# Kernel tuning notes

Hardware: AMD Instinct MI355X
Metric: run time of the kernel (lower is better)

## Reference

```python
import jax, jax.numpy as jnp
import numpy as np

B, N, DIM_IN, DIM, DIM_C, RES, PAD, NBLK = 4, 32768, 3, 128, 128, 64, 0.1, 5
R2 = RES * RES
PLANES = ((0, 2), (0, 1), (1, 2))  # xz, xy, yz as in ConvONet


def setup_inputs() -> dict:
    key = jax.random.key(0)
    ks = jax.random.split(key, 8)
    x = jax.random.uniform(ks[0], (B, N, DIM_IN), minval=-0.55, maxval=0.55, dtype=jnp.float32)
    w = lambda k, sh: (jax.random.normal(k, sh, dtype=jnp.float32) * 0.02)
    return {
        "x": x,
        "stem_w": w(ks[1], (DIM_IN, 2 * DIM)), "stem_b": jnp.zeros((2 * DIM,), jnp.float32),
        "blk_fc0_w": w(ks[2], (NBLK, 2 * DIM, DIM)), "blk_fc0_b": jnp.zeros((NBLK, DIM), jnp.float32),
        "blk_fc1_w": w(ks[3], (NBLK, DIM, DIM)), "blk_fc1_b": jnp.zeros((NBLK, DIM), jnp.float32),
        "blk_sc_w": w(ks[4], (NBLK, 2 * DIM, DIM)), "blk_sc_b": jnp.zeros((NBLK, DIM), jnp.float32),
        "fc_c_w": w(ks[5], (DIM, DIM_C)), "fc_c_b": jnp.zeros((DIM_C,), jnp.float32),
    }


def _tri_indices(xyz):
    # per-plane flat grid index, ConvONet-style normalization with padding
    idxs = []
    for (a, b) in PLANES:
        p = xyz[..., (a, b)] / (1.0 + PAD + 1e-3) + 0.5
        p = jnp.clip(p, 0.0, 1.0 - 1e-6)
        ij = jnp.clip((p * RES).astype(jnp.int32), 0, RES - 1)
        idxs.append(ij[..., 0] + RES * ij[..., 1])  # (B, N)
    return idxs


def _scatter(c, idx, reduction):
    # c: (B, N, D), idx: (B, N) -> (B, R2, D)
    b, n, d = c.shape
    seg = (idx + jnp.arange(b, dtype=idx.dtype)[:, None] * R2).reshape(-1)
    flat = c.reshape(b * n, d)
    if reduction == "max":
        out = jax.ops.segment_max(flat, seg, num_segments=b * R2)
        out = jnp.where(jnp.isfinite(out), out, jnp.zeros((), c.dtype))  # empty cells -> 0
    else:  # mean
        s = jax.ops.segment_sum(flat, seg, num_segments=b * R2)
        cnt = jax.ops.segment_sum(jnp.ones((b * n, 1), c.dtype), seg, num_segments=b * R2)
        out = s / jnp.maximum(cnt, 1.0)
    return out.reshape(b, R2, d)


def _pool_local(h, idxs):
    # scatter-max into each triplane, gather back per-point, sum over the 3 planes
    out = jnp.zeros_like(h)
    for idx in idxs:
        grid = _scatter(h, idx, "max")                       # (B, R2, D)
        out = out + jnp.take_along_axis(grid, idx[..., None], axis=1)
    return out


def _block(h, w0, b0, w1, b1, ws, bs):
    # pre-activation residual MLP (ResnetBlockFC)
    net = jax.nn.relu(h) @ w0 + b0
    dx = jax.nn.relu(net) @ w1 + b1
    return h @ ws + bs + dx


def reference(x, stem_w, stem_b, blk_fc0_w, blk_fc0_b, blk_fc1_w, blk_fc1_b,
              blk_sc_w, blk_sc_b, fc_c_w, fc_c_b):
    xyz = x[..., :3]
    idxs = _tri_indices(xyz)
    h = x @ stem_w + stem_b                                  # (B, N, 2*DIM)
    h = _block(h, blk_fc0_w[0], blk_fc0_b[0], blk_fc1_w[0], blk_fc1_b[0], blk_sc_w[0], blk_sc_b[0])
    for i in range(1, NBLK):
        h = jnp.concatenate([h, _pool_local(h, idxs)], axis=-1)
        h = _block(h, blk_fc0_w[i], blk_fc0_b[i], blk_fc1_w[i], blk_fc1_b[i], blk_sc_w[i], blk_sc_b[i])
    c = h @ fc_c_w + fc_c_b                                  # (B, N, DIM_C)
    tri = jnp.stack([_scatter(c, idx, "mean") for idx in idxs])  # (3, B, R2, DIM_C)
    # flat index = i + RES*j -> reshape gives (j, i); move channels to front
    tri = tri.reshape(3, B, RES, RES, DIM_C).transpose(0, 1, 4, 2, 3)  # (3, B, DIM_C, RES, RES)
    return (xyz, c, tri)
```

## Files before the change

### kernel.cpp

```cpp
#include <hip/hip_runtime.h>
#include <hip/hip_bf16.h>

#define B_   4
#define NPTS 32768
#define BN   131072
#define RES  64
#define R2   4096
#define DIM  128
#define K2   256
#define NBLK 5
#define NSEG (3*B_*R2)

typedef __bf16 bf16x8 __attribute__((ext_vector_type(8)));
typedef float  f32x16 __attribute__((ext_vector_type(16)));
typedef unsigned int uintv4 __attribute__((ext_vector_type(4)));

#define MFMA(a,b,c) __builtin_amdgcn_mfma_f32_32x32x16_bf16((a),(b),(c),0,0,0)

#define O_IDX  0
#define O_CNT  (O_IDX + BN*16)
#define O_OFF  (O_CNT + NSEG*4)
#define O_WOFF (O_OFF + NSEG*4)
#define O_LIST (O_WOFF + NSEG*4)
#define O_H    (O_LIST + 3*BN*4)
#define O_GRID (O_H + BN*DIM*2)
#define O_W    (O_GRID + NSEG*DIM*2)
#define WBLK_ELEMS 81920

#define OUT_C_OFF   393216
#define OUT_TRI_OFF 17170432

__device__ __forceinline__ unsigned short f2bf(float f){
  unsigned int u = __float_as_uint(f);
  return (unsigned short)((u + 0x7fffu + ((u >> 16) & 1u)) >> 16);
}
__device__ __forceinline__ float bflo(unsigned int u){ return __uint_as_float(u << 16); }
__device__ __forceinline__ float bfhi(unsigned int u){ return __uint_as_float(u & 0xffff0000u); }
__device__ __forceinline__ int coord_bin(float u){
  float p = u / 1.101f + 0.5f;
  p = fminf(fmaxf(p, 0.0f), (float)(1.0 - 1e-6));
  int i = (int)(p * 64.0f);
  return i < 0 ? 0 : (i > 63 ? 63 : i);
}
__device__ __forceinline__ unsigned int pk_relu(unsigned int a){
  unsigned int r, z = 0;
  asm("v_pk_max_f16 %0, %1, %2" : "=v"(r) : "v"(a), "v"(z));
  return r;
}
__device__ __forceinline__ bf16x8 relu8(bf16x8 v){
  uintv4 u = __builtin_bit_cast(uintv4, v);
  u[0] = pk_relu(u[0]); u[1] = pk_relu(u[1]); u[2] = pk_relu(u[2]); u[3] = pk_relu(u[3]);
  return __builtin_bit_cast(bf16x8, u);
}

__global__ void k_prep(const float* __restrict__ x, float* __restrict__ out_xyz,
                       int* __restrict__ idx4, int* __restrict__ cnt){
  int p = blockIdx.x * 256 + threadIdx.x;
  if (p >= BN) return;
  float x0 = x[p*3+0], x1 = x[p*3+1], x2 = x[p*3+2];
  out_xyz[p*3+0] = x0; out_xyz[p*3+1] = x1; out_xyz[p*3+2] = x2;
  int b = p >> 15;
  int c0 = coord_bin(x0) + 64*coord_bin(x2);
  int c1 = coord_bin(x0) + 64*coord_bin(x1);
  int c2 = coord_bin(x1) + 64*coord_bin(x2);
  int4 c4; c4.x = c0; c4.y = c1; c4.z = c2; c4.w = 0;
  *(int4*)(idx4 + p*4) = c4;
  atomicAdd(&cnt[(0*B_+b)*R2 + c0], 1);
  atomicAdd(&cnt[(1*B_+b)*R2 + c1], 1);
  atomicAdd(&cnt[(2*B_+b)*R2 + c2], 1);
}

__global__ __launch_bounds__(1024) void k_scan(const int* __restrict__ cnt,
                                               int* __restrict__ off, int* __restrict__ woff){
  __shared__ int part[1024];
  const int t = threadIdx.x;
  const int PER = NSEG / 1024;
  const int base = t * PER;
  int s = 0;
  for (int i = 0; i < PER; ++i) s += cnt[base+i];
  part[t] = s;
  __syncthreads();
  for (int d = 1; d < 1024; d <<= 1){
    int v = (t >= d) ? part[t-d] : 0;
    __syncthreads();
    part[t] += v;
    __syncthreads();
  }
  int acc = (t == 0) ? 0 : part[t-1];
  for (int i = 0; i < PER; ++i){
    int c = cnt[base+i];
    off[base+i] = acc; woff[base+i] = acc;
    acc += c;
  }
}

__global__ void k_bin(const int* __restrict__ idx4, int* __restrict__ woff, int* __restrict__ list){
  int p = blockIdx.x * 256 + threadIdx.x;
  if (p >= BN) return;
  int b = p >> 15;
  int4 c4 = *(const int4*)(idx4 + p*4);
  int cs[3] = {c4.x, c4.y, c4.z};
  #pragma unroll
  for (int pl = 0; pl < 3; ++pl){
    int s = (pl*B_+b)*R2 + cs[pl];
    int slot = atomicAdd(&woff[s], 1);
    list[slot] = p;
  }
}

__global__ void k_prepw(const float* __restrict__ fc0, const float* __restrict__ fc1,
                        const float* __restrict__ scw, const float* __restrict__ fcc,
                        unsigned short* __restrict__ wdst){
  int t = blockIdx.x * 256 + threadIdx.x;
  if (t < 163840){
    int b = t >> 15, r = t & 32767;
    int j = r & 7, l = (r >> 3) & 63, ks = (r >> 9) & 15, w = r >> 13;
    int n = w*32 + (l & 31);
    int k = ks*16 + (l >> 5)*8 + j;
    wdst[b*WBLK_ELEMS + r] = f2bf(fc0[(b*256 + k)*128 + n]);
  } else if (t < 327680){
    int t2 = t - 163840;
    int b = t2 >> 15, r = t2 & 32767;
    int j = r & 7, l = (r >> 3) & 63, ks = (r >> 9) & 15, w = r >> 13;
    int n = w*32 + (l & 31);
    int k = ks*16 + (l >> 5)*8 + j;
    wdst[b*WBLK_ELEMS + 32768 + r] = f2bf(scw[(b*256 + k)*128 + n]);
  } else if (t < 409600){
    int t2 = t - 327680;
    int b = t2 >> 14, r = t2 & 16383;
    int j = r & 7, l = (r >> 3) & 63, ks = (r >> 9) & 7, w = (r >> 12) & 3;
    int n = w*32 + (l & 31);
    int k = ks*16 + (l >> 5)*8 + j;
    wdst[b*WBLK_ELEMS + 65536 + r] = f2bf(fc1[(b*128 + k)*128 + n]);
  } else if (t < 425984){
    int r = t - 409600;
    int j = r & 7, l = (r >> 3) & 63, ks = (r >> 9) & 7, w = (r >> 12) & 3;
    int n = w*32 + (l & 31);
    int k = ks*16 + (l >> 5)*8 + j;
    wdst[5*WBLK_ELEMS + r] = f2bf(fcc[k*128 + n]);
  }
}

__global__ __launch_bounds__(256) void k_cellmax(const unsigned short* __restrict__ h,
    const int* __restrict__ off, const int* __restrict__ cnt,
    const int* __restrict__ list, unsigned short* __restrict__ gbf){
  const int seg = (blockIdx.x * 256 + threadIdx.x) >> 6;
  const int l = threadIdx.x & 63;
  const int base = off[seg], n = cnt[seg];
  float m0 = -INFINITY, m1 = -INFINITY;
  int i = 0;
  for (; i + 4 <= n; i += 4){
    int p0 = list[base+i], p1 = list[base+i+1], p2 = list[base+i+2], p3 = list[base+i+3];
    unsigned int u0 = *(const unsigned int*)(h + p0*DIM + 2*l);
    unsigned int u1 = *(const unsigned int*)(h + p1*DIM + 2*l);
    unsigned int u2 = *(const unsigned int*)(h + p2*DIM + 2*l);
    unsigned int u3 = *(const unsigned int*)(h + p3*DIM + 2*l);
    m0 = fmaxf(fmaxf(fmaxf(m0, bflo(u0)), fmaxf(bflo(u1), bflo(u2))), bflo(u3));
    m1 = fmaxf(fmaxf(fmaxf(m1, bfhi(u0)), fmaxf(bfhi(u1), bfhi(u2))), bfhi(u3));
  }
  for (; i < n; ++i){
    int p = list[base+i];
    unsigned int u = *(const unsigned int*)(h + p*DIM + 2*l);
    m0 = fmaxf(m0, bflo(u)); m1 = fmaxf(m1, bfhi(u));
  }
  unsigned int o = 0;
  if (n > 0) o = (__float_as_uint(m0) >> 16) | (__float_as_uint(m1) & 0xffff0000u);
  *(unsigned int*)(gbf + (size_t)seg*DIM + 2*l) = o;
}

template<int MODE>
__global__ __launch_bounds__(256, 4) void k_block(
    const float* __restrict__ x,
    const float* __restrict__ stem_w, const float* __restrict__ stem_b,
    unsigned short* __restrict__ h,
    const unsigned short* __restrict__ gbf, const int* __restrict__ idx4,
    const unsigned short* __restrict__ wT,
    const float* __restrict__ b0g, const float* __restrict__ b1g, const float* __restrict__ bsg)
{
  __shared__ unsigned short lh2[64*256];
  const int t = threadIdx.x;
  const int tile0 = blockIdx.x * 64;

  if (MODE == 0){
    const int dg8 = (t & 31) * 8;
    const int prow = t >> 5;
    float wa[8], wb[8], wc[8], bb[8];
    #pragma unroll
    for (int j = 0; j < 8; ++j){
      wa[j] = stem_w[dg8+j]; wb[j] = stem_w[256+dg8+j]; wc[j] = stem_w[512+dg8+j];
      bb[j] = stem_b[dg8+j];
    }
    #pragma unroll
    for (int pass = 0; pass < 8; ++pass){
      int p = prow + pass*8;
      int pg = tile0 + p;
      float x0 = x[pg*3+0], x1 = x[pg*3+1], x2 = x[pg*3+2];
      unsigned int pk[4];
      #pragma unroll
      for (int j = 0; j < 4; ++j){
        float v0 = bb[2*j]   + x0*wa[2*j]   + x1*wb[2*j]   + x2*wc[2*j];
        float v1 = bb[2*j+1] + x0*wa[2*j+1] + x1*wb[2*j+1] + x2*wc[2*j+1];
        pk[j] = (unsigned int)f2bf(v0) | ((unsigned int)f2bf(v1) << 16);
      }
      uint4 q; q.x = pk[0]; q.y = pk[1]; q.z = pk[2]; q.w = pk[3];
      *(uint4*)((char*)lh2 + p*512 + ((dg8*2) ^ ((p & 7) << 4))) = q;
    }
  } else {
    const int dg4 = (t & 31) * 4;
    const int prow = t >> 5;
    int4 cl[8];
    #pragma unroll
    for (int pass = 0; pass < 8; ++pass)
      cl[pass] = *(const int4*)(idx4 + (tile0 + prow + pass*8)*4);
    #pragma unroll
    for (int pass = 0; pass < 8; ++pass){
      int p = prow + pass*8;
      int pg = tile0 + p;
      int b = pg >> 15;
      uint2 hv = *(const uint2*)(h + pg*DIM + dg4);
      const unsigned short* g0 = gbf + ((size_t)((0*B_+b)*R2 + cl[pass].x))*DIM + dg4;
      const unsigned short* g1 = gbf + ((size_t)((1*B_+b)*R2 + cl[pass].y))*DIM + dg4;
      const unsigned short* g2 = gbf + ((size_t)((2*B_+b)*R2 + cl[pass].z))*DIM + dg4;
      uint2 v0 = *(const uint2*)g0;
      uint2 v1 = *(const uint2*)g1;
      uint2 v2 = *(const uint2*)g2;
      *(uint2*)((char*)lh2 + p*512 + ((dg4*2) ^ ((p & 7) << 4))) = hv;
      float s0 = bflo(v0.x) + bflo(v1.x) + bflo(v2.x);
      float s1 = bfhi(v0.x) + bfhi(v1.x) + bfhi(v2.x);
      float s2 = bflo(v0.y) + bflo(v1.y) + bflo(v2.y);
      float s3 = bfhi(v0.y) + bfhi(v1.y) + bfhi(v2.y);
      uint2 pv;
      pv.x = (unsigned int)f2bf(s0) | ((unsigned int)f2bf(s1) << 16);
      pv.y = (unsigned int)f2bf(s2) | ((unsigned int)f2bf(s3) << 16);
      *(uint2*)((char*)lh2 + p*512 + (((128 + dg4)*2) ^ ((p & 7) << 4))) = pv;
    }
  }
  __syncthreads();

  const int w  = t >> 6;
  const int l  = t & 63;
  const int lm = l & 31;
  const int hi = l >> 5;
  const int D0 = w * 32;
  const int swz  = (lm & 7) << 4;
  const unsigned short* w0f = wT +          ((size_t)w*16*64 + l)*8;
  const unsigned short* wsf = wT + 32768 +  ((size_t)w*16*64 + l)*8;
  const unsigned short* w1f = wT + 65536 +  ((size_t)w* 8*64 + l)*8;

  f32x16 an0, an1, as0, as1;
  #pragma unroll
  for (int i = 0; i < 16; ++i){ an0[i] = 0.f; an1[i] = 0.f; as0[i] = 0.f; as1[i] = 0.f; }

  const char* lr0 = (const char*)lh2 + lm*512;
  const char* lr1 = (const char*)lh2 + (32+lm)*512;

  #pragma unroll 4
  for (int ks = 0; ks < 16; ++ks){
    bf16x8 a0 = *(const bf16x8*)(w0f + ks*512);
    bf16x8 a1 = *(const bf16x8*)(wsf + ks*512);
    int kb = (ks*32 + hi*16) ^ swz;
    bf16x8 br0 = *(const bf16x8*)(lr0 + kb);
    bf16x8 br1 = *(const bf16x8*)(lr1 + kb);
    an0 = MFMA(a0, relu8(br0), an0);
    as0 = MFMA(a1, br0, as0);
    an1 = MFMA(a0, relu8(br1), an1);
    as1 = MFMA(a1, br1, as1);
  }

  __syncthreads();

  {
    char* nr0 = (char*)lh2 + lm*256;
    char* nr1 = (char*)lh2 + (32+lm)*256;
    #pragma unroll
    for (int g = 0; g < 4; ++g){
      int d0 = D0 + 8*g + 4*hi;
      float q0 = b0g[d0], q1 = b0g[d0+1], q2 = b0g[d0+2], q3 = b0g[d0+3];
      uint2 u0, u1;
      {
        float v0 = fmaxf(an0[4*g+0]+q0, 0.f), v1 = fmaxf(an0[4*g+1]+q1, 0.f);
        float v2 = fmaxf(an0[4*g+2]+q2, 0.f), v3 = fmaxf(an0[4*g+3]+q3, 0.f);
        u0.x = (unsigned int)f2bf(v0) | ((unsigned int)f2bf(v1) << 16);
        u0.y = (unsigned int)f2bf(v2) | ((unsigned int)f2bf(v3) << 16);
      }
      {
        float v0 = fmaxf(an1[4*g+0]+q0, 0.f), v1 = fmaxf(an1[4*g+1]+q1, 0.f);
        float v2 = fmaxf(an1[4*g+2]+q2, 0.f), v3 = fmaxf(an1[4*g+3]+q3, 0.f);
        u1.x = (unsigned int)f2bf(v0) | ((unsigned int)f2bf(v1) << 16);
        u1.y = (unsigned int)f2bf(v2) | ((unsigned int)f2bf(v3) << 16);
      }
      int ob = (d0*2) ^ swz;
      *(uint2*)(nr0 + ob) = u0;
      *(uint2*)(nr1 + ob) = u1;
    }
  }
  __syncthreads();

  f32x16 ad0, ad1;
  #pragma unroll
  for (int i = 0; i < 16; ++i){ ad0[i] = 0.f; ad1[i] = 0.f; }
  const char* nr0c = (const char*)lh2 + lm*256;
  const char* nr1c = (const char*)lh2 + (32+lm)*256;
  #pragma unroll 4
  for (int ks = 0; ks < 8; ++ks){
    bf16x8 a = *(const bf16x8*)(w1f + ks*512);
    int kb = (ks*32 + hi*16) ^ swz;
    ad0 = MFMA(a, *(const bf16x8*)(nr0c + kb), ad0);
    ad1 = MFMA(a, *(const bf16x8*)(nr1c + kb), ad1);
  }

  #pragma unroll
  for (int g = 0; g < 4; ++g){
    int d0 = D0 + 8*g + 4*hi;
    float p0 = b1g[d0]   + bsg[d0];
    float p1 = b1g[d0+1] + bsg[d0+1];
    float p2 = b1g[d0+2] + bsg[d0+2];
    float p3 = b1g[d0+3] + bsg[d0+3];
    {
      int pg = tile0 + lm;
      float v0 = as0[4*g+0]+ad0[4*g+0]+p0, v1 = as0[4*g+1]+ad0[4*g+1]+p1;
      float v2 = as0[4*g+2]+ad0[4*g+2]+p2, v3 = as0[4*g+3]+ad0[4*g+3]+p3;
      uint2 o;
      o.x = (unsigned int)f2bf(v0) | ((unsigned int)f2bf(v1) << 16);
      o.y = (unsigned int)f2bf(v2) | ((unsigned int)f2bf(v3) << 16);
      *(uint2*)(h + pg*DIM + d0) = o;
    }
    {
      int pg = tile0 + 32 + lm;
      float v0 = as1[4*g+0]+ad1[4*g+0]+p0, v1 = as1[4*g+1]+ad1[4*g+1]+p1;
      float v2 = as1[4*g+2]+ad1[4*g+2]+p2, v3 = as1[4*g+3]+ad1[4*g+3]+p3;
      uint2 o;
      o.x = (unsigned int)f2bf(v0) | ((unsigned int)f2bf(v1) << 16);
      o.y = (unsigned int)f2bf(v2) | ((unsigned int)f2bf(v3) << 16);
      *(uint2*)(h + pg*DIM + d0) = o;
    }
  }
}

__global__ __launch_bounds__(256) void k_final(
    const unsigned short* __restrict__ h,
    const unsigned short* __restrict__ fcf, const float* __restrict__ fcb,
    float* __restrict__ cout)
{
  __shared__ unsigned short lh[64*128];
  const int t = threadIdx.x;
  const int tile0 = blockIdx.x * 64;
  {
    int dg4 = (t & 31) * 4, prow = t >> 5;
    #pragma unroll
    for (int pass = 0; pass < 8; ++pass){
      int p = prow + pass*8, pg = tile0 + p;
      uint2 hv = *(const uint2*)(h + pg*DIM + dg4);
      *(uint2*)((char*)lh + p*256 + ((dg4*2) ^ ((p & 7) << 4))) = hv;
    }
  }
  __syncthreads();
  const int w = t >> 6, l = t & 63, lm = l & 31, hi = l >> 5;
  const int D0 = w*32, swz = (lm & 7) << 4;
  const unsigned short* fw = fcf + ((size_t)w*8*64 + l)*8;
  f32x16 ac0, ac1;
  #pragma unroll
  for (int i = 0; i < 16; ++i){ ac0[i] = 0.f; ac1[i] = 0.f; }
  const char* r0 = (const char*)lh + lm*256;
  const char* r1 = (const char*)lh + (32+lm)*256;
  #pragma unroll 4
  for (int ks = 0; ks < 8; ++ks){
    bf16x8 a = *(const bf16x8*)(fw + ks*512);
    int kb = (ks*32 + hi*16) ^ swz;
    ac0 = MFMA(a, *(const bf16x8*)(r0 + kb), ac0);
    ac1 = MFMA(a, *(const bf16x8*)(r1 + kb), ac1);
  }
  #pragma unroll
  for (int g = 0; g < 4; ++g){
    int d0 = D0 + 8*g + 4*hi;
    float q0 = fcb[d0], q1 = fcb[d0+1], q2 = fcb[d0+2], q3 = fcb[d0+3];
    {
      int pg = tile0 + lm;
      float4 f4;
      f4.x = ac0[4*g+0]+q0; f4.y = ac0[4*g+1]+q1; f4.z = ac0[4*g+2]+q2; f4.w = ac0[4*g+3]+q3;
      *(float4*)(cout + (size_t)pg*DIM + d0) = f4;
    }
    {
      int pg = tile0 + 32 + lm;
      float4 f4;
      f4.x = ac1[4*g+0]+q0; f4.y = ac1[4*g+1]+q1; f4.z = ac1[4*g+2]+q2; f4.w = ac1[4*g+3]+q3;
      *(float4*)(cout + (size_t)pg*DIM + d0) = f4;
    }
  }
}

__global__ __launch_bounds__(256) void k_cellmean(const unsigned short* __restrict__ h,
    const int* __restrict__ off, const int* __restrict__ cnt,
    const int* __restrict__ list, unsigned short* __restrict__ mgrid){
  const int seg = (blockIdx.x * 256 + threadIdx.x) >> 6;
  const int l = threadIdx.x & 63;
  const int base = off[seg], n = cnt[seg];
  float s0 = 0.f, s1 = 0.f;
  int i = 0;
  for (; i + 4 <= n; i += 4){
    int p0 = list[base+i], p1 = list[base+i+1], p2 = list[base+i+2], p3 = list[base+i+3];
    unsigned int u0 = *(const unsigned int*)(h + p0*DIM + 2*l);
    unsigned int u1 = *(const unsigned int*)(h + p1*DIM + 2*l);
    unsigned int u2 = *(const unsigned int*)(h + p2*DIM + 2*l);
    unsigned int u3 = *(const unsigned int*)(h + p3*DIM + 2*l);
    s0 += (bflo(u0) + bflo(u1)) + (bflo(u2) + bflo(u3));
    s1 += (bfhi(u0) + bfhi(u1)) + (bfhi(u2) + bfhi(u3));
  }
  for (; i < n; ++i){
    int p = list[base+i];
    unsigned int u = *(const unsigned int*)(h + p*DIM + 2*l);
    s0 += bflo(u); s1 += bfhi(u);
  }
  float den = 1.0f / (float)(n < 1 ? 1 : n);
  unsigned int o = (unsigned int)f2bf(s0 * den) | ((unsigned int)f2bf(s1 * den) << 16);
  *(unsigned int*)(mgrid + (size_t)seg*DIM + 2*l) = o;
}

__global__ __launch_bounds__(256) void k_trigemm(const unsigned short* __restrict__ mgrid,
    const unsigned short* __restrict__ fcf, const float* __restrict__ fcb,
    const int* __restrict__ cnt, float* __restrict__ tri)
{
  __shared__ unsigned short lh[64*128];
  const int t = threadIdx.x;
  const int wg = blockIdx.x;
  const int pl = wg >> 8;
  const int b  = (wg >> 6) & 3;
  const int r  = wg & 63;
  const int segbase = (pl*B_+b)*R2 + r*64;
  {
    int dg4 = (t & 31) * 4, prow = t >> 5;
    #pragma unroll
    for (int pass = 0; pass < 8; ++pass){
      int p = prow + pass*8;
      uint2 hv = *(const uint2*)(mgrid + (size_t)(segbase + p)*DIM + dg4);
      *(uint2*)((char*)lh + p*256 + ((dg4*2) ^ ((p & 7) << 4))) = hv;
    }
  }
  __syncthreads();
  const int w = t >> 6, l = t & 63, lm = l & 31, hi = l >> 5;
  const int D0 = w*32, swz = (lm & 7) << 4;
  const unsigned short* fw = fcf + ((size_t)w*8*64 + l)*8;
  f32x16 ac0, ac1;
  #pragma unroll
  for (int i = 0; i < 16; ++i){ ac0[i] = 0.f; ac1[i] = 0.f; }
  const char* r0 = (const char*)lh + lm*256;
  const char* r1 = (const char*)lh + (32+lm)*256;
  #pragma unroll 4
  for (int ks = 0; ks < 8; ++ks){
    bf16x8 a = *(const bf16x8*)(fw + ks*512);
    int kb = (ks*32 + hi*16) ^ swz;
    ac0 = MFMA(a, *(const bf16x8*)(r0 + kb), ac0);
    ac1 = MFMA(a, *(const bf16x8*)(r1 + kb), ac1);
  }
  float z0 = (cnt[segbase + lm]      > 0) ? 1.0f : 0.0f;
  float z1 = (cnt[segbase + 32 + lm] > 0) ? 1.0f : 0.0f;
  float* dst = tri + ((size_t)((pl*B_+b)*DIM)) * R2 + r*64;
  #pragma unroll
  for (int g = 0; g < 4; ++g){
    int d0 = D0 + 8*g + 4*hi;
    #pragma unroll
    for (int j = 0; j < 4; ++j){
      int d = d0 + j;
      float q = fcb[d];
      dst[(size_t)d*R2 + lm]      = (ac0[4*g+j] + q) * z0;
      dst[(size_t)d*R2 + 32 + lm] = (ac1[4*g+j] + q) * z1;
    }
  }
}

extern "C" void kernel_launch(void* const* d_in, const int* in_sizes, int n_in,
                              void* d_out, int out_size, void* d_ws, size_t ws_size,
                              hipStream_t stream){
  const float* x      = (const float*)d_in[0];
  const float* stem_w = (const float*)d_in[1];
  const float* stem_b = (const float*)d_in[2];
  const float* fc0_w  = (const float*)d_in[3];
  const float* fc0_b  = (const float*)d_in[4];
  const float* fc1_w  = (const float*)d_in[5];
  const float* fc1_b  = (const float*)d_in[6];
  const float* sc_w   = (const float*)d_in[7];
  const float* sc_b   = (const float*)d_in[8];
  const float* fcc_w  = (const float*)d_in[9];
  const float* fcc_b  = (const float*)d_in[10];

  char* ws = (char*)d_ws;
  int* idx4           = (int*)(ws + O_IDX);
  int* cnt            = (int*)(ws + O_CNT);
  int* off            = (int*)(ws + O_OFF);
  int* woff           = (int*)(ws + O_WOFF);
  int* list           = (int*)(ws + O_LIST);
  unsigned short* h   = (unsigned short*)(ws + O_H);
  unsigned short* gbf = (unsigned short*)(ws + O_GRID);
  unsigned short* wbf = (unsigned short*)(ws + O_W);

  float* out     = (float*)d_out;
  float* out_xyz = out;
  float* out_c   = out + OUT_C_OFF;
  float* out_tri = out + OUT_TRI_OFF;

  hipMemsetAsync(cnt, 0, NSEG*4, stream);
  k_prep<<<BN/256, 256, 0, stream>>>(x, out_xyz, idx4, cnt);
  k_prepw<<<1664, 256, 0, stream>>>(fc0_w, fc1_w, sc_w, fcc_w, wbf);
  k_scan<<<1, 1024, 0, stream>>>(cnt, off, woff);
  k_bin<<<BN/256, 256, 0, stream>>>(idx4, woff, list);

  k_block<0><<<BN/64, 256, 0, stream>>>(x, stem_w, stem_b, h, nullptr, nullptr,
                                        wbf, fc0_b, fc1_b, sc_b);
  for (int i = 1; i < NBLK; ++i){
    k_cellmax<<<NSEG/4, 256, 0, stream>>>(h, off, cnt, list, gbf);
    k_block<1><<<BN/64, 256, 0, stream>>>(nullptr, nullptr, nullptr, h, gbf, idx4,
                                          wbf + (size_t)i*WBLK_ELEMS,
                                          fc0_b + i*DIM, fc1_b + i*DIM, sc_b + i*DIM);
  }
  k_final<<<BN/64, 256, 0, stream>>>(h, wbf + (size_t)5*WBLK_ELEMS, fcc_b, out_c);
  k_cellmean<<<NSEG/4, 256, 0, stream>>>(h, off, cnt, list, gbf);
  k_trigemm<<<768, 256, 0, stream>>>(gbf, wbf + (size_t)5*WBLK_ELEMS, fcc_b, cnt, out_tri);
}
```

Baseline: 422.2 us.

## Double k_block point tile to 128 to reuse weight fragments across more MFMAs

The residual block kernel now processes 128 points per workgroup instead of 64. Each wave keeps four accumulator sets per GEMM, so every weight fragment loaded from global memory feeds twice as many MFMAs. The change raises LDS use to 64KB per block and roughly doubles accumulator registers, so launch bounds drop to 2 blocks per CU. The cell-index prefetch into registers is removed, and the index is now loaded inside the gather loop.

```diff
diff --git a/kernel.cpp b/kernel.cpp
--- a/kernel.cpp
+++ b/kernel.cpp
@@ -10,6 +10,7 @@
 #define K2   256
 #define NBLK 5
 #define NSEG (3*B_*R2)
+#define TILE 128
 
 typedef __bf16 bf16x8 __attribute__((ext_vector_type(8)));
 typedef float  f32x16 __attribute__((ext_vector_type(16)));
@@ -169,7 +170,7 @@
 }
 
 template<int MODE>
-__global__ __launch_bounds__(256, 4) void k_block(
+__global__ __launch_bounds__(256, 2) void k_block(
     const float* __restrict__ x,
     const float* __restrict__ stem_w, const float* __restrict__ stem_b,
     unsigned short* __restrict__ h,
@@ -177,9 +178,9 @@
     const unsigned short* __restrict__ wT,
     const float* __restrict__ b0g, const float* __restrict__ b1g, const float* __restrict__ bsg)
 {
-  __shared__ unsigned short lh2[64*256];
+  __shared__ unsigned short lh2[TILE*256];
   const int t = threadIdx.x;
-  const int tile0 = blockIdx.x * 64;
+  const int tile0 = blockIdx.x * TILE;
 
   if (MODE == 0){
     const int dg8 = (t & 31) * 8;
@@ -191,7 +192,7 @@
       bb[j] = stem_b[dg8+j];
     }
     #pragma unroll
-    for (int pass = 0; pass < 8; ++pass){
+    for (int pass = 0; pass < 16; ++pass){
       int p = prow + pass*8;
       int pg = tile0 + p;
       float x0 = x[pg*3+0], x1 = x[pg*3+1], x2 = x[pg*3+2];
@@ -208,19 +209,16 @@
   } else {
     const int dg4 = (t & 31) * 4;
     const int prow = t >> 5;
-    int4 cl[8];
-    #pragma unroll
-    for (int pass = 0; pass < 8; ++pass)
-      cl[pass] = *(const int4*)(idx4 + (tile0 + prow + pass*8)*4);
-    #pragma unroll
-    for (int pass = 0; pass < 8; ++pass){
+    #pragma unroll
+    for (int pass = 0; pass < 16; ++pass){
       int p = prow + pass*8;
       int pg = tile0 + p;
       int b = pg >> 15;
+      int4 c4 = *(const int4*)(idx4 + pg*4);
       uint2 hv = *(const uint2*)(h + pg*DIM + dg4);
-      const unsigned short* g0 = gbf + ((size_t)((0*B_+b)*R2 + cl[pass].x))*DIM + dg4;
-      const unsigned short* g1 = gbf + ((size_t)((1*B_+b)*R2 + cl[pass].y))*DIM + dg4;
-      const unsigned short* g2 = gbf + ((size_t)((2*B_+b)*R2 + cl[pass].z))*DIM + dg4;
+      const unsigned short* g0 = gbf + ((size_t)((0*B_+b)*R2 + c4.x))*DIM + dg4;
+      const unsigned short* g1 = gbf + ((size_t)((1*B_+b)*R2 + c4.y))*DIM + dg4;
+      const unsigned short* g2 = gbf + ((size_t)((2*B_+b)*R2 + c4.z))*DIM + dg4;
       uint2 v0 = *(const uint2*)g0;
       uint2 v1 = *(const uint2*)g1;
       uint2 v2 = *(const uint2*)g2;
@@ -247,12 +245,17 @@
   const unsigned short* wsf = wT + 32768 +  ((size_t)w*16*64 + l)*8;
   const unsigned short* w1f = wT + 65536 +  ((size_t)w* 8*64 + l)*8;
 
-  f32x16 an0, an1, as0, as1;
-  #pragma unroll
-  for (int i = 0; i < 16; ++i){ an0[i] = 0.f; an1[i] = 0.f; as0[i] = 0.f; as1[i] = 0.f; }
-
-  const char* lr0 = (const char*)lh2 + lm*512;
+  f32x16 an0, an1, an2, an3, as0, as1, as2, as3;
+  #pragma unroll
+  for (int i = 0; i < 16; ++i){
+    an0[i]=0.f; an1[i]=0.f; an2[i]=0.f; an3[i]=0.f;
+    as0[i]=0.f; as1[i]=0.f; as2[i]=0.f; as3[i]=0.f;
+  }
+
+  const char* lr0 = (const char*)lh2 + ( 0+lm)*512;
   const char* lr1 = (const char*)lh2 + (32+lm)*512;
+  const char* lr2 = (const char*)lh2 + (64+lm)*512;
+  const char* lr3 = (const char*)lh2 + (96+lm)*512;
 
   #pragma unroll 4
   for (int ks = 0; ks < 16; ++ks){
@@ -261,52 +264,63 @@
     int kb = (ks*32 + hi*16) ^ swz;
     bf16x8 br0 = *(const bf16x8*)(lr0 + kb);
     bf16x8 br1 = *(const bf16x8*)(lr1 + kb);
-    an0 = MFMA(a0, relu8(br0), an0);
-    as0 = MFMA(a1, br0, as0);
-    an1 = MFMA(a0, relu8(br1), an1);
-    as1 = MFMA(a1, br1, as1);
+    bf16x8 br2 = *(const bf16x8*)(lr2 + kb);
+    bf16x8 br3 = *(const bf16x8*)(lr3 + kb);
+    an0 = MFMA(a0, relu8(br0), an0);  as0 = MFMA(a1, br0, as0);
+    an1 = MFMA(a0, relu8(br1), an1);  as1 = MFMA(a1, br1, as1);
+    an2 = MFMA(a0, relu8(br2), an2);  as2 = MFMA(a1, br2, as2);
+    an3 = MFMA(a0, relu8(br3), an3);  as3 = MFMA(a1, br3, as3);
   }
 
   __syncthreads();
 
   {
-    char* nr0 = (char*)lh2 + lm*256;
+    char* nr0 = (char*)lh2 + ( 0+lm)*256;
     char* nr1 = (char*)lh2 + (32+lm)*256;
+    char* nr2 = (char*)lh2 + (64+lm)*256;
+    char* nr3 = (char*)lh2 + (96+lm)*256;
     #pragma unroll
     for (int g = 0; g < 4; ++g){
       int d0 = D0 + 8*g + 4*hi;
       float q0 = b0g[d0], q1 = b0g[d0+1], q2 = b0g[d0+2], q3 = b0g[d0+3];
-      uint2 u0, u1;
-      {
-        float v0 = fmaxf(an0[4*g+0]+q0, 0.f), v1 = fmaxf(an0[4*g+1]+q1, 0.f);
-        float v2 = fmaxf(an0[4*g+2]+q2, 0.f), v3 = fmaxf(an0[4*g+3]+q3, 0.f);
-        u0.x = (unsigned int)f2bf(v0) | ((unsigned int)f2bf(v1) << 16);
-        u0.y = (unsigned int)f2bf(v2) | ((unsigned int)f2bf(v3) << 16);
-      }
-      {
-        float v0 = fmaxf(an1[4*g+0]+q0, 0.f), v1 = fmaxf(an1[4*g+1]+q1, 0.f);
-        float v2 = fmaxf(an1[4*g+2]+q2, 0.f), v3 = fmaxf(an1[4*g+3]+q3, 0.f);
-        u1.x = (unsigned int)f2bf(v0) | ((unsigned int)f2bf(v1) << 16);
-        u1.y = (unsigned int)f2bf(v2) | ((unsigned int)f2bf(v3) << 16);
-      }
       int ob = (d0*2) ^ swz;
-      *(uint2*)(nr0 + ob) = u0;
-      *(uint2*)(nr1 + ob) = u1;
+      uint2 u;
+      float v0,v1,v2,v3;
+      v0=fmaxf(an0[4*g+0]+q0,0.f); v1=fmaxf(an0[4*g+1]+q1,0.f);
+      v2=fmaxf(an0[4*g+2]+q2,0.f); v3=fmaxf(an0[4*g+3]+q3,0.f);
+      u.x=(unsigned)f2bf(v0)|((unsigned)f2bf(v1)<<16); u.y=(unsigned)f2bf(v2)|((unsigned)f2bf(v3)<<16);
+      *(uint2*)(nr0 + ob) = u;
+      v0=fmaxf(an1[4*g+0]+q0,0.f); v1=fmaxf(an1[4*g+1]+q1,0.f);
+      v2=fmaxf(an1[4*g+2]+q2,0.f); v3=fmaxf(an1[4*g+3]+q3,0.f);
+      u.x=(unsigned)f2bf(v0)|((unsigned)f2bf(v1)<<16); u.y=(unsigned)f2bf(v2)|((unsigned)f2bf(v3)<<16);
+      *(uint2*)(nr1 + ob) = u;
+      v0=fmaxf(an2[4*g+0]+q0,0.f); v1=fmaxf(an2[4*g+1]+q1,0.f);
+      v2=fmaxf(an2[4*g+2]+q2,0.f); v3=fmaxf(an2[4*g+3]+q3,0.f);
+      u.x=(unsigned)f2bf(v0)|((unsigned)f2bf(v1)<<16); u.y=(unsigned)f2bf(v2)|((unsigned)f2bf(v3)<<16);
+      *(uint2*)(nr2 + ob) = u;
+      v0=fmaxf(an3[4*g+0]+q0,0.f); v1=fmaxf(an3[4*g+1]+q1,0.f);
+      v2=fmaxf(an3[4*g+2]+q2,0.f); v3=fmaxf(an3[4*g+3]+q3,0.f);
+      u.x=(unsigned)f2bf(v0)|((unsigned)f2bf(v1)<<16); u.y=(unsigned)f2bf(v2)|((unsigned)f2bf(v3)<<16);
+      *(uint2*)(nr3 + ob) = u;
     }
   }
   __syncthreads();
 
-  f32x16 ad0, ad1;
-  #pragma unroll
-  for (int i = 0; i < 16; ++i){ ad0[i] = 0.f; ad1[i] = 0.f; }
-  const char* nr0c = (const char*)lh2 + lm*256;
-  const char* nr1c = (const char*)lh2 + (32+lm)*256;
+  f32x16 ad0, ad1, ad2, ad3;
+  #pragma unroll
+  for (int i = 0; i < 16; ++i){ ad0[i]=0.f; ad1[i]=0.f; ad2[i]=0.f; ad3[i]=0.f; }
+  const char* nc0 = (const char*)lh2 + ( 0+lm)*256;
+  const char* nc1 = (const char*)lh2 + (32+lm)*256;
+  const char* nc2 = (const char*)lh2 + (64+lm)*256;
+  const char* nc3 = (const char*)lh2 + (96+lm)*256;
   #pragma unroll 4
   for (int ks = 0; ks < 8; ++ks){
     bf16x8 a = *(const bf16x8*)(w1f + ks*512);
     int kb = (ks*32 + hi*16) ^ swz;
-    ad0 = MFMA(a, *(const bf16x8*)(nr0c + kb), ad0);
-    ad1 = MFMA(a, *(const bf16x8*)(nr1c + kb), ad1);
+    ad0 = MFMA(a, *(const bf16x8*)(nc0 + kb), ad0);
+    ad1 = MFMA(a, *(const bf16x8*)(nc1 + kb), ad1);
+    ad2 = MFMA(a, *(const bf16x8*)(nc2 + kb), ad2);
+    ad3 = MFMA(a, *(const bf16x8*)(nc3 + kb), ad3);
   }
 
   #pragma unroll
@@ -316,24 +330,24 @@
     float p1 = b1g[d0+1] + bsg[d0+1];
     float p2 = b1g[d0+2] + bsg[d0+2];
     float p3 = b1g[d0+3] + bsg[d0+3];
-    {
-      int pg = tile0 + lm;
-      float v0 = as0[4*g+0]+ad0[4*g+0]+p0, v1 = as0[4*g+1]+ad0[4*g+1]+p1;
-      float v2 = as0[4*g+2]+ad0[4*g+2]+p2, v3 = as0[4*g+3]+ad0[4*g+3]+p3;
-      uint2 o;
-      o.x = (unsigned int)f2bf(v0) | ((unsigned int)f2bf(v1) << 16);
-      o.y = (unsigned int)f2bf(v2) | ((unsigned int)f2bf(v3) << 16);
-      *(uint2*)(h + pg*DIM + d0) = o;
-    }
-    {
-      int pg = tile0 + 32 + lm;
-      float v0 = as1[4*g+0]+ad1[4*g+0]+p0, v1 = as1[4*g+1]+ad1[4*g+1]+p1;
-      float v2 = as1[4*g+2]+ad1[4*g+2]+p2, v3 = as1[4*g+3]+ad1[4*g+3]+p3;
-      uint2 o;
-      o.x = (unsigned int)f2bf(v0) | ((unsigned int)f2bf(v1) << 16);
-      o.y = (unsigned int)f2bf(v2) | ((unsigned int)f2bf(v3) << 16);
-      *(uint2*)(h + pg*DIM + d0) = o;
-    }
+    uint2 o;
+    float v0,v1,v2,v3;
+    v0=as0[4*g+0]+ad0[4*g+0]+p0; v1=as0[4*g+1]+ad0[4*g+1]+p1;
+    v2=as0[4*g+2]+ad0[4*g+2]+p2; v3=as0[4*g+3]+ad0[4*g+3]+p3;
+    o.x=(unsigned)f2bf(v0)|((unsigned)f2bf(v1)<<16); o.y=(unsigned)f2bf(v2)|((unsigned)f2bf(v3)<<16);
+    *(uint2*)(h + (tile0 +  0 + lm)*DIM + d0) = o;
+    v0=as1[4*g+0]+ad1[4*g+0]+p0; v1=as1[4*g+1]+ad1[4*g+1]+p1;
+    v2=as1[4*g+2]+ad1[4*g+2]+p2; v3=as1[4*g+3]+ad1[4*g+3]+p3;
+    o.x=(unsigned)f2bf(v0)|((unsigned)f2bf(v1)<<16); o.y=(unsigned)f2bf(v2)|((unsigned)f2bf(v3)<<16);
+    *(uint2*)(h + (tile0 + 32 + lm)*DIM + d0) = o;
+    v0=as2[4*g+0]+ad2[4*g+0]+p0; v1=as2[4*g+1]+ad2[4*g+1]+p1;
+    v2=as2[4*g+2]+ad2[4*g+2]+p2; v3=as2[4*g+3]+ad2[4*g+3]+p3;
+    o.x=(unsigned)f2bf(v0)|((unsigned)f2bf(v1)<<16); o.y=(unsigned)f2bf(v2)|((unsigned)f2bf(v3)<<16);
+    *(uint2*)(h + (tile0 + 64 + lm)*DIM + d0) = o;
+    v0=as3[4*g+0]+ad3[4*g+0]+p0; v1=as3[4*g+1]+ad3[4*g+1]+p1;
+    v2=as3[4*g+2]+ad3[4*g+2]+p2; v3=as3[4*g+3]+ad3[4*g+3]+p3;
+    o.x=(unsigned)f2bf(v0)|((unsigned)f2bf(v1)<<16); o.y=(unsigned)f2bf(v2)|((unsigned)f2bf(v3)<<16);
+    *(uint2*)(h + (tile0 + 96 + lm)*DIM + d0) = o;
   }
 }
 
@@ -504,13 +518,13 @@
   k_scan<<<1, 1024, 0, stream>>>(cnt, off, woff);
   k_bin<<<BN/256, 256, 0, stream>>>(idx4, woff, list);
 
-  k_block<0><<<BN/64, 256, 0, stream>>>(x, stem_w, stem_b, h, nullptr, nullptr,
-                                        wbf, fc0_b, fc1_b, sc_b);
+  k_block<0><<<BN/TILE, 256, 0, stream>>>(x, stem_w, stem_b, h, nullptr, nullptr,
+                                          wbf, fc0_b, fc1_b, sc_b);
   for (int i = 1; i < NBLK; ++i){
     k_cellmax<<<NSEG/4, 256, 0, stream>>>(h, off, cnt, list, gbf);
-    k_block<1><<<BN/64, 256, 0, stream>>>(nullptr, nullptr, nullptr, h, gbf, idx4,
-                                          wbf + (size_t)i*WBLK_ELEMS,
-                                          fc0_b + i*DIM, fc1_b + i*DIM, sc_b + i*DIM);
+    k_block<1><<<BN/TILE, 256, 0, stream>>>(nullptr, nullptr, nullptr, h, gbf, idx4,
+                                            wbf + (size_t)i*WBLK_ELEMS,
+                                            fc0_b + i*DIM, fc1_b + i*DIM, sc_b + i*DIM);
   }
   k_final<<<BN/64, 256, 0, stream>>>(h, wbf + (size_t)5*WBLK_ELEMS, fcc_b, out_c);
   k_cellmean<<<NSEG/4, 256, 0, stream>>>(h, off, cnt, list, gbf);
```

Result: slower. 441.0 us (+4.5%).
